# Kernel tuning notes

Hardware: AMD Instinct MI355X
Metric: run time of the kernel (lower is better)

The kernel has to match this reference:

```python
import jax, jax.numpy as jnp
import numpy as np

B, S, H, MID = 8, 2048, 256, 32


def get_rotary_matrix(s, d):
    # Faithful to llama-from-scratch get_rotary_matrix: theta = 10000**(-2*(i-1)/d)
    pos = jnp.arange(s, dtype=jnp.float32)
    i = jnp.arange(d // 2, dtype=jnp.float32)
    theta = 10000.0 ** (-2.0 * (i - 1.0) / d)
    ang = pos[:, None] * theta[None, :]            # [s, d/2]
    c, sn = jnp.cos(ang), jnp.sin(ang)
    ev = 2 * jnp.arange(d // 2)
    od = ev + 1
    R = jnp.zeros((s, d, d), jnp.float32)
    R = R.at[:, ev, ev].set(c).at[:, od, od].set(c)
    R = R.at[:, ev, od].set(-sn).at[:, od, ev].set(sn)
    return R


def setup_inputs() -> dict:
    key = jax.random.key(0)
    ks = jax.random.split(key, 7)
    sc = 0.02
    x = jax.random.normal(ks[0], (B, S, H), jnp.float32)
    # nn.Linear weights: l1.weight [mid, in], l2.weight [out, mid]; y = x @ W.T
    wq1 = jax.random.normal(ks[1], (MID, H), jnp.float32) * sc
    wq2 = jax.random.normal(ks[2], (H, MID), jnp.float32) * sc
    wk1 = jax.random.normal(ks[3], (MID, H), jnp.float32) * sc
    wk2 = jax.random.normal(ks[4], (H, MID), jnp.float32) * sc
    wv1 = jax.random.normal(ks[5], (MID, H), jnp.float32) * sc
    wv2 = jax.random.normal(ks[6], (H, MID), jnp.float32) * sc
    r = get_rotary_matrix(S, H)                    # [S, H, H] buffer
    return {"x": x, "r": r, "wq1": wq1, "wq2": wq2, "wk1": wk1,
            "wk2": wk2, "wv1": wv1, "wv2": wv2}


def reference(x, r, wq1, wq2, wk1, wk2, wv1, wv2):
    b, s, h = x.shape
    q = (x @ wq1.T) @ wq2.T                        # LoRA q: [b,s,h]
    k = (x @ wk1.T) @ wk2.T
    v = (x @ wv1.T) @ wv2.T
    # RoPE as dense per-position rotation matmul (bmm over seq dim)
    qr = jnp.einsum('bsh,shk->bsk', q, r[:s])
    kr = jnp.einsum('bsh,shk->bsk', k, r[:s])
    attn = jnp.einsum('bqh,bkh->bqk', qr, kr) * (h ** -0.5)   # [b,s,s]
    mask = jnp.tril(jnp.ones((s, s), bool))
    attn = jnp.where(mask, attn, -jnp.inf)
    attn = jax.nn.softmax(attn, axis=-1)
    out = attn @ v                                 # [b,s,h]
    return out
```

## Files before the change

kernel.cpp:

```cpp
#include <hip/hip_runtime.h>
#include <hip/hip_bf16.h>
#include <math.h>

typedef float f32x4 __attribute__((ext_vector_type(4)));
typedef float f32x16 __attribute__((ext_vector_type(16)));
typedef unsigned int u32x4 __attribute__((ext_vector_type(4)));
typedef __bf16 bf16x8 __attribute__((ext_vector_type(8)));
typedef unsigned short u16;

#define MFMA16(acc, a, b)                                              \
  acc = __builtin_amdgcn_mfma_f32_16x16x32_bf16(                       \
      __builtin_bit_cast(bf16x8, a), __builtin_bit_cast(bf16x8, b),    \
      acc, 0, 0, 0)

#define MFMA32(acc, a, b)                                              \
  acc = __builtin_amdgcn_mfma_f32_32x32x16_bf16(                       \
      __builtin_bit_cast(bf16x8, a), __builtin_bit_cast(bf16x8, b),    \
      acc, 0, 0, 0)

#define GLOAD_LDS16(gp, lp)                                            \
  __builtin_amdgcn_global_load_lds(                                    \
      (const __attribute__((address_space(1))) void*)(const void*)(gp),\
      (__attribute__((address_space(3))) void*)(void*)(lp), 16, 0, 0)

__device__ __forceinline__ u16 f2bf(float f) {
  union { float f; unsigned u; } v; v.f = f;
  unsigned r = v.u + 0x7FFFu + ((v.u >> 16) & 1u);
  return (u16)(r >> 16);
}

__device__ __forceinline__ float b2f(u16 h) {
  union { unsigned u; float f; } v; v.u = ((unsigned)h) << 16; return v.f;
}

__device__ __forceinline__ unsigned cvtpk(float lo, float hi) {
  unsigned r;
  asm("v_cvt_pk_bf16_f32 %0, %1, %2" : "=v"(r) : "v"(lo), "v"(hi));
  return r;
}

#define BFEX(vec, e) ((u16)(((e) & 1) ? ((vec)[(e) >> 1] >> 16) : ((vec)[(e) >> 1] & 0xffffu)))

__global__ __launch_bounds__(256) void cs_kernel(float2* __restrict__ cs) {
  int idx = blockIdx.x * 256 + threadIdx.x;
  int s = idx >> 7, j = idx & 127;
  float theta = powf(10000.f, (2.f - 2.f * (float)j) * (1.f / 256.f));
  float ang = (float)s * theta;
  float sn, c;
  sincosf(ang, &sn, &c);
  cs[idx] = make_float2(c, sn);
}

__global__ __launch_bounds__(256) void proj_kernel(
    const float* __restrict__ x,
    const float* __restrict__ w1q, const float* __restrict__ w2q,
    const float* __restrict__ w1k, const float* __restrict__ w2k,
    const float* __restrict__ w1v, const float* __restrict__ w2v,
    const float2* __restrict__ cs,
    u16* __restrict__ qout, u16* __restrict__ kout, u16* __restrict__ vout)
{
  __shared__ __align__(16) u16 xs[64 * 256];
  __shared__ __align__(16) u16 w1s[32 * 256];
  __shared__ __align__(16) u16 w2s[256 * 40];
  __shared__ __align__(16) u16 tls[64 * 40];
  __shared__ __align__(16) u16 bnc[64 * 264];

  const int tid = threadIdx.x;
  const int w = tid >> 6, l = tid & 63;
  const int l15 = l & 15, lg = l >> 4;
  const int row0 = blockIdx.x * 64;

  #pragma unroll
  for (int i = 0; i < 16; ++i) {
    int idx = tid + 256 * i;
    int r = idx >> 6, c4 = idx & 63;
    float4 v = reinterpret_cast<const float4*>(x)[(size_t)(row0 + r) * 64 + c4];
    int ci = (c4 * 4) ^ ((r & 7) << 3);
    *reinterpret_cast<ushort4*>(&xs[r * 256 + ci]) =
        make_ushort4(f2bf(v.x), f2bf(v.y), f2bf(v.z), f2bf(v.w));
  }

  const float* W1[3] = {w1q, w1k, w1v};
  const float* W2[3] = {w2q, w2k, w2v};
  u16* OUT[3] = {qout, kout, vout};

  for (int p = 0; p < 3; ++p) {
    __syncthreads();
    const float* w1 = W1[p];
    const float* w2 = W2[p];
    #pragma unroll
    for (int i = 0; i < 8; ++i) {
      int idx = tid + 256 * i;
      int r = idx >> 6, c4 = idx & 63;
      float4 v = reinterpret_cast<const float4*>(w1)[idx];
      int ci = (c4 * 4) ^ ((r & 7) << 3);
      *reinterpret_cast<ushort4*>(&w1s[r * 256 + ci]) =
          make_ushort4(f2bf(v.x), f2bf(v.y), f2bf(v.z), f2bf(v.w));
    }
    #pragma unroll
    for (int i = 0; i < 8; ++i) {
      int idx = tid + 256 * i;
      int r = idx >> 3, c4 = idx & 7;
      float4 v = reinterpret_cast<const float4*>(w2)[idx];
      *reinterpret_cast<ushort4*>(&w2s[r * 40 + c4 * 4]) =
          make_ushort4(f2bf(v.x), f2bf(v.y), f2bf(v.z), f2bf(v.w));
    }
    __syncthreads();

    f32x4 acc0 = {0.f, 0.f, 0.f, 0.f}, acc1 = {0.f, 0.f, 0.f, 0.f};
    {
      const int arow = w * 16 + l15;
      #pragma unroll
      for (int kk = 0; kk < 8; ++kk) {
        u32x4 a = *reinterpret_cast<const u32x4*>(
            &xs[arow * 256 + ((kk * 32 + lg * 8) ^ ((arow & 7) << 3))]);
        const int b0r = l15, b1r = l15 + 16;
        u32x4 b0 = *reinterpret_cast<const u32x4*>(
            &w1s[b0r * 256 + ((kk * 32 + lg * 8) ^ ((b0r & 7) << 3))]);
        u32x4 b1 = *reinterpret_cast<const u32x4*>(
            &w1s[b1r * 256 + ((kk * 32 + lg * 8) ^ ((b1r & 7) << 3))]);
        MFMA16(acc0, a, b0);
        MFMA16(acc1, a, b1);
      }
    }
    #pragma unroll
    for (int rr = 0; rr < 4; ++rr) {
      int trow = w * 16 + lg * 4 + rr;
      tls[trow * 40 + l15]      = f2bf(acc0[rr]);
      tls[trow * 40 + 16 + l15] = f2bf(acc1[rr]);
    }

    f32x4 yac[16];
    #pragma unroll
    for (int oc = 0; oc < 16; ++oc) yac[oc] = (f32x4){0.f, 0.f, 0.f, 0.f};
    {
      u32x4 a = *reinterpret_cast<const u32x4*>(&tls[(w * 16 + l15) * 40 + lg * 8]);
      #pragma unroll
      for (int oc = 0; oc < 16; ++oc) {
        u32x4 b = *reinterpret_cast<const u32x4*>(&w2s[(oc * 16 + l15) * 40 + lg * 8]);
        MFMA16(yac[oc], a, b);
      }
    }

    #pragma unroll
    for (int oc = 0; oc < 16; ++oc)
      #pragma unroll
      for (int rr = 0; rr < 4; ++rr)
        bnc[(w * 16 + lg * 4 + rr) * 264 + oc * 16 + l15] = f2bf(yac[oc][rr]);
    __syncthreads();

    {
      const int frow = tid >> 2, c0 = (tid & 3) * 64;
      const int grow = row0 + frow;
      const int sidx = grow & 2047;
      u16* outp = OUT[p];
      const float2* csr = cs + ((size_t)sidx << 7) + (c0 >> 1);
      const bool dorope = (p < 2);
      #pragma unroll
      for (int seg = 0; seg < 8; ++seg) {
        u32x4 v8 = *reinterpret_cast<const u32x4*>(&bnc[frow * 264 + c0 + seg * 8]);
        u32x4 res = v8;
        if (dorope) {
          #pragma unroll
          for (int j = 0; j < 4; ++j) {
            float ev = b2f(BFEX(v8, 2 * j)), od = b2f(BFEX(v8, 2 * j + 1));
            float2 cv = csr[seg * 4 + j];
            u16 re = f2bf(ev * cv.x + od * cv.y);
            u16 ro = f2bf(od * cv.x - ev * cv.y);
            res[j] = ((unsigned)ro << 16) | (unsigned)re;
          }
        }
        *reinterpret_cast<u32x4*>(&outp[(size_t)grow * 256 + c0 + seg * 8]) = res;
      }
    }
  }
}

__global__ __launch_bounds__(256, 2) void attn_kernel(
    const u16* __restrict__ qg, const u16* __restrict__ kg,
    const u16* __restrict__ vg, u16* __restrict__ po,
    float* __restrict__ pmw, float* __restrict__ plw)
{
  __shared__ __align__(16) u16 ks2[2][32 * 256];
  __shared__ __align__(16) u16 vt2[2][256 * 40];
  __shared__ float paxw[4][32];

  const int tid = threadIdx.x;
  const int w = tid >> 6, l = tid & 63;
  const int s = w >> 1, h2 = w & 1;
  const int q31 = l & 31, g = l >> 5;

  const int bx = blockIdx.x;
  const int bb = bx & 7;
  const int o_ = bx >> 3;
  const int idx = (o_ < 32) ? o_ : 95 - o_;
  const int qt = 31 - (idx >> 1);
  const int hv = idx & 1;
  const int tmx = 2 * qt + 1;

  const int qbase = qt * 64;
  const size_t boff = (size_t)bb * (2048 * 256);
  const int qg_ = qbase + s * 32 + q31;

  u32x4 qf[16];
  {
    const u16* qp = qg + boff + (size_t)qg_ * 256 + g * 8;
    #pragma unroll
    for (int st = 0; st < 16; ++st)
      qf[st] = *reinterpret_cast<const u32x4*>(qp + st * 16);
  }

  f32x16 o[4];
  #pragma unroll
  for (int dt = 0; dt < 4; ++dt)
    #pragma unroll
    for (int r = 0; r < 16; ++r) o[dt][r] = 0.f;
  float m_run = -INFINITY, l_run = 0.f;

  const int vc = tid & 31;
  const int kvr = (tid >> 5) * 4;
  const int swv = (vc & 3) << 3;
  const int swr = (q31 >> 3) << 3;
  const int ksw = (q31 & 7) << 3;
  const int kbase = q31 * 256;

  const u16* kgb = kg + boff;
  const u16* vgb = vg + boff;

  {
    const u16* kp = kgb + (size_t)(hv * 32) * 256;
    #pragma unroll
    for (int j = 0; j < 4; ++j) {
      int i2 = tid + 256 * j;
      int r = i2 >> 5, c8 = (i2 & 31) * 8;
      GLOAD_LDS16(kp + r * 256 + (c8 ^ ((r & 7) << 3)), &ks2[0][i2 * 8]);
    }
    const u16* vp = vgb + (size_t)(hv * 32) * 256;
    u32x4 vq[4];
    #pragma unroll
    for (int j = 0; j < 4; ++j)
      vq[j] = *reinterpret_cast<const u32x4*>(vp + (size_t)(kvr + j) * 256 + vc * 8);
    #pragma unroll
    for (int e = 0; e < 8; ++e) {
      int d = vc * 8 + e;
      *reinterpret_cast<ushort4*>(&vt2[0][d * 40 + (kvr ^ swv)]) =
          make_ushort4(BFEX(vq[0], e), BFEX(vq[1], e), BFEX(vq[2], e), BFEX(vq[3], e));
    }
  }
  __syncthreads();

  int cur = 0;
  for (int t = hv; t <= tmx; t += 2) {
    const int kv0 = t * 32;
    const int nb = cur ^ 1;
    const bool pf = (t + 2 <= tmx);

    u32x4 vq[4];
    if (pf) {
      const u16* kp = kgb + (size_t)((t + 2) * 32) * 256;
      #pragma unroll
      for (int j = 0; j < 4; ++j) {
        int i2 = tid + 256 * j;
        int r = i2 >> 5, c8 = (i2 & 31) * 8;
        GLOAD_LDS16(kp + r * 256 + (c8 ^ ((r & 7) << 3)), &ks2[nb][i2 * 8]);
      }
      const u16* vp = vgb + (size_t)((t + 2) * 32) * 256;
      #pragma unroll
      for (int j = 0; j < 4; ++j)
        vq[j] = *reinterpret_cast<const u32x4*>(vp + (size_t)(kvr + j) * 256 + vc * 8);
    }

    f32x16 sca, scb;
    #pragma unroll
    for (int r = 0; r < 16; ++r) { sca[r] = 0.f; scb[r] = 0.f; }
    #pragma unroll
    for (int st = 0; st < 8; ++st) {
      u32x4 a0 = *reinterpret_cast<const u32x4*>(
          &ks2[cur][kbase + ((st * 32 + g * 8) ^ ksw)]);
      u32x4 a1 = *reinterpret_cast<const u32x4*>(
          &ks2[cur][kbase + ((st * 32 + 16 + g * 8) ^ ksw)]);
      MFMA32(sca, a0, qf[2 * st]);
      MFMA32(scb, a1, qf[2 * st + 1]);
    }

    f32x16 sc;
    #pragma unroll
    for (int r = 0; r < 16; ++r) sc[r] = (sca[r] + scb[r]) * 0.0625f;
    if (kv0 + 31 > qbase + s * 32) {
      #pragma unroll
      for (int r = 0; r < 16; ++r) {
        int kvg = kv0 + (r & 3) + 8 * (r >> 2) + 4 * g;
        if (kvg > qg_) sc[r] = -INFINITY;
      }
    }
    float red[8];
    #pragma unroll
    for (int i = 0; i < 8; ++i) red[i] = fmaxf(sc[i], sc[i + 8]);
    #pragma unroll
    for (int i = 0; i < 4; ++i) red[i] = fmaxf(red[i], red[i + 4]);
    float mx = fmaxf(fmaxf(red[0], red[1]), fmaxf(red[2], red[3]));
    mx = fmaxf(mx, __shfl_xor(mx, 32, 64));
    float mnew = fmaxf(m_run, mx);
    float msafe = fmaxf(mnew, -1e30f);
    float alpha = __expf(m_run - msafe);
    m_run = mnew;
    #pragma unroll
    for (int r = 0; r < 16; ++r) sc[r] = __expf(sc[r] - msafe);
    #pragma unroll
    for (int i = 0; i < 8; ++i) red[i] = sc[i] + sc[i + 8];
    #pragma unroll
    for (int i = 0; i < 4; ++i) red[i] = red[i] + red[i + 4];
    float lh = (red[0] + red[1]) + (red[2] + red[3]);
    lh += __shfl_xor(lh, 32, 64);
    l_run = l_run * alpha + lh;

    unsigned wv[8], xw[8];
    #pragma unroll
    for (int j = 0; j < 8; ++j) wv[j] = cvtpk(sc[2 * j], sc[2 * j + 1]);
    #pragma unroll
    for (int j = 0; j < 8; ++j) xw[j] = __shfl_xor(wv[j], 32, 64);
    u32x4 pa0, pa1;
    pa0[0] = g ? xw[2] : wv[0]; pa0[1] = g ? xw[3] : wv[1];
    pa0[2] = g ? wv[2] : xw[0]; pa0[3] = g ? wv[3] : xw[1];
    pa1[0] = g ? xw[6] : wv[4]; pa1[1] = g ? xw[7] : wv[5];
    pa1[2] = g ? wv[6] : xw[4]; pa1[3] = g ? wv[7] : xw[5];

    if (l < 32) paxw[w][l] = alpha;
    f32x4 aR[4];
    #pragma unroll
    for (int i = 0; i < 4; ++i)
      aR[i] = *reinterpret_cast<const f32x4*>(&paxw[w][i * 8 + 4 * g]);
    #pragma unroll
    for (int dt = 0; dt < 4; ++dt)
      #pragma unroll
      for (int r = 0; r < 16; ++r) o[dt][r] *= aR[r >> 2][r & 3];

    #pragma unroll
    for (int dt = 0; dt < 4; ++dt) {
      int rb = (h2 * 128 + dt * 32 + q31) * 40;
      u32x4 b0 = *reinterpret_cast<const u32x4*>(&vt2[cur][rb + ((g * 8) ^ swr)]);
      u32x4 b1 = *reinterpret_cast<const u32x4*>(&vt2[cur][rb + ((16 + g * 8) ^ swr)]);
      MFMA32(o[dt], pa0, b0);
      MFMA32(o[dt], pa1, b1);
    }

    if (pf) {
      #pragma unroll
      for (int e = 0; e < 8; ++e) {
        int d = vc * 8 + e;
        *reinterpret_cast<ushort4*>(&vt2[nb][d * 40 + (kvr ^ swv)]) =
            make_ushort4(BFEX(vq[0], e), BFEX(vq[1], e), BFEX(vq[2], e), BFEX(vq[3], e));
      }
    }
    __syncthreads();
    cur ^= 1;
  }

  const int pidx = (bb * 32 + qt) * 2 + hv;
  u16* op = po + (size_t)pidx * (64 * 256);
  #pragma unroll
  for (int dt = 0; dt < 4; ++dt) {
    #pragma unroll
    for (int r = 0; r < 16; ++r) {
      int row = s * 32 + (r & 3) + 8 * (r >> 2) + 4 * g;
      int col = h2 * 128 + dt * 32 + q31;
      op[(size_t)row * 256 + col] = f2bf(o[dt][r]);
    }
  }
  if (h2 == 0 && l < 32) {
    pmw[pidx * 64 + s * 32 + l] = m_run;
    plw[pidx * 64 + s * 32 + l] = l_run;
  }
}

__global__ __launch_bounds__(256) void combine_kernel(
    const u16* __restrict__ po, const float* __restrict__ pm,
    const float* __restrict__ plv, float* __restrict__ outg)
{
  int idx = blockIdx.x * 256 + threadIdx.x;
  int d8 = idx & 31;
  int row = idx >> 5;
  int bb = row >> 11, qrem = row & 2047;
  int qt = qrem >> 6, r64 = qrem & 63;
  int p0 = (bb * 32 + qt) * 2;

  float m0 = pm[p0 * 64 + r64], m1 = pm[(p0 + 1) * 64 + r64];
  float l0 = plv[p0 * 64 + r64], l1 = plv[(p0 + 1) * 64 + r64];
  float mm = fmaxf(m0, m1);
  float w0 = __expf(m0 - mm), w1 = __expf(m1 - mm);
  float inv = 1.f / (l0 * w0 + l1 * w1);

  u32x4 a0 = *reinterpret_cast<const u32x4*>(
      po + (size_t)p0 * (64 * 256) + (size_t)r64 * 256 + d8 * 8);
  u32x4 a1 = *reinterpret_cast<const u32x4*>(
      po + (size_t)(p0 + 1) * (64 * 256) + (size_t)r64 * 256 + d8 * 8);
  f32x4 r0, r1;
  #pragma unroll
  for (int e = 0; e < 4; ++e)
    r0[e] = (b2f(BFEX(a0, e)) * w0 + b2f(BFEX(a1, e)) * w1) * inv;
  #pragma unroll
  for (int e = 0; e < 4; ++e)
    r1[e] = (b2f(BFEX(a0, e + 4)) * w0 + b2f(BFEX(a1, e + 4)) * w1) * inv;
  float* op = outg + (size_t)row * 256 + d8 * 8;
  *reinterpret_cast<f32x4*>(op) = r0;
  *reinterpret_cast<f32x4*>(op + 4) = r1;
}

extern "C" void kernel_launch(void* const* d_in, const int* in_sizes, int n_in,
                              void* d_out, int out_size, void* d_ws, size_t ws_size,
                              hipStream_t stream) {
  const float* x   = (const float*)d_in[0];
  const float* wq1 = (const float*)d_in[2];
  const float* wq2 = (const float*)d_in[3];
  const float* wk1 = (const float*)d_in[4];
  const float* wk2 = (const float*)d_in[5];
  const float* wv1 = (const float*)d_in[6];
  const float* wv2 = (const float*)d_in[7];

  const size_t NTOK = (size_t)8 * 2048;
  u16* qw = (u16*)d_ws;
  u16* kw = qw + NTOK * 256;
  u16* vw = kw + NTOK * 256;
  float2* cs = (float2*)(vw + NTOK * 256);
  u16* po    = (u16*)(cs + 2048 * 128);
  float* pm  = (float*)(po + (size_t)512 * 64 * 256);
  float* plv = pm + 512 * 64;

  cs_kernel<<<1024, 256, 0, stream>>>(cs);
  proj_kernel<<<256, 256, 0, stream>>>(x, wq1, wq2, wk1, wk2, wv1, wv2,
                                       cs, qw, kw, vw);
  attn_kernel<<<512, 256, 0, stream>>>(qw, kw, vw, po, pm, plv);
  combine_kernel<<<2048, 256, 0, stream>>>(po, pm, plv, (float*)d_out);
}
```

Baseline: 109.1 us.

## Split KV into four strided partitions with atomic work-queue scheduling in attention

The attention kernel becomes persistent. Each block pulls work items from a per-batch atomic counter, which is reset in cs_kernel, and the item order runs longest tiles first. The KV range of each query tile is split four ways instead of two, and the combine kernel merges four partial softmax results. It also skips the output rescale when alpha equals 1 across the wave. This is meant to improve load balance in causal attention, at the cost of more partial-output traffic, a larger combine step and atomic/sync overhead per item.

```diff
diff --git a/kernel.cpp b/kernel.cpp
--- a/kernel.cpp
+++ b/kernel.cpp
@@ -41,8 +41,10 @@
 
 #define BFEX(vec, e) ((u16)(((e) & 1) ? ((vec)[(e) >> 1] >> 16) : ((vec)[(e) >> 1] & 0xffffu)))
 
-__global__ __launch_bounds__(256) void cs_kernel(float2* __restrict__ cs) {
+__global__ __launch_bounds__(256) void cs_kernel(float2* __restrict__ cs,
+                                                 int* __restrict__ ctr) {
   int idx = blockIdx.x * 256 + threadIdx.x;
+  if (blockIdx.x == 0 && threadIdx.x < 8) ctr[threadIdx.x] = 0;
   int s = idx >> 7, j = idx & 127;
   float theta = powf(10000.f, (2.f - 2.f * (float)j) * (1.f / 256.f));
   float ang = (float)s * theta;
@@ -179,43 +181,22 @@
 __global__ __launch_bounds__(256, 2) void attn_kernel(
     const u16* __restrict__ qg, const u16* __restrict__ kg,
     const u16* __restrict__ vg, u16* __restrict__ po,
-    float* __restrict__ pmw, float* __restrict__ plw)
+    float* __restrict__ pmw, float* __restrict__ plw, int* __restrict__ ctr)
 {
   __shared__ __align__(16) u16 ks2[2][32 * 256];
   __shared__ __align__(16) u16 vt2[2][256 * 40];
   __shared__ float paxw[4][32];
+  __shared__ int s_item;
 
   const int tid = threadIdx.x;
   const int w = tid >> 6, l = tid & 63;
   const int s = w >> 1, h2 = w & 1;
   const int q31 = l & 31, g = l >> 5;
 
-  const int bx = blockIdx.x;
-  const int bb = bx & 7;
-  const int o_ = bx >> 3;
-  const int idx = (o_ < 32) ? o_ : 95 - o_;
-  const int qt = 31 - (idx >> 1);
-  const int hv = idx & 1;
-  const int tmx = 2 * qt + 1;
-
-  const int qbase = qt * 64;
+  const int bb = blockIdx.x & 7;
   const size_t boff = (size_t)bb * (2048 * 256);
-  const int qg_ = qbase + s * 32 + q31;
-
-  u32x4 qf[16];
-  {
-    const u16* qp = qg + boff + (size_t)qg_ * 256 + g * 8;
-    #pragma unroll
-    for (int st = 0; st < 16; ++st)
-      qf[st] = *reinterpret_cast<const u32x4*>(qp + st * 16);
-  }
-
-  f32x16 o[4];
-  #pragma unroll
-  for (int dt = 0; dt < 4; ++dt)
-    #pragma unroll
-    for (int r = 0; r < 16; ++r) o[dt][r] = 0.f;
-  float m_run = -INFINITY, l_run = 0.f;
+  const u16* kgb = kg + boff;
+  const u16* vgb = vg + boff;
 
   const int vc = tid & 31;
   const int kvr = (tid >> 5) * 4;
@@ -224,152 +205,182 @@
   const int ksw = (q31 & 7) << 3;
   const int kbase = q31 * 256;
 
-  const u16* kgb = kg + boff;
-  const u16* vgb = vg + boff;
-
-  {
-    const u16* kp = kgb + (size_t)(hv * 32) * 256;
-    #pragma unroll
-    for (int j = 0; j < 4; ++j) {
-      int i2 = tid + 256 * j;
-      int r = i2 >> 5, c8 = (i2 & 31) * 8;
-      GLOAD_LDS16(kp + r * 256 + (c8 ^ ((r & 7) << 3)), &ks2[0][i2 * 8]);
-    }
-    const u16* vp = vgb + (size_t)(hv * 32) * 256;
-    u32x4 vq[4];
-    #pragma unroll
-    for (int j = 0; j < 4; ++j)
-      vq[j] = *reinterpret_cast<const u32x4*>(vp + (size_t)(kvr + j) * 256 + vc * 8);
-    #pragma unroll
-    for (int e = 0; e < 8; ++e) {
-      int d = vc * 8 + e;
-      *reinterpret_cast<ushort4*>(&vt2[0][d * 40 + (kvr ^ swv)]) =
-          make_ushort4(BFEX(vq[0], e), BFEX(vq[1], e), BFEX(vq[2], e), BFEX(vq[3], e));
-    }
-  }
-  __syncthreads();
-
-  int cur = 0;
-  for (int t = hv; t <= tmx; t += 2) {
-    const int kv0 = t * 32;
-    const int nb = cur ^ 1;
-    const bool pf = (t + 2 <= tmx);
-
-    u32x4 vq[4];
-    if (pf) {
-      const u16* kp = kgb + (size_t)((t + 2) * 32) * 256;
-      #pragma unroll
-      for (int j = 0; j < 4; ++j) {
-        int i2 = tid + 256 * j;
-        int r = i2 >> 5, c8 = (i2 & 31) * 8;
-        GLOAD_LDS16(kp + r * 256 + (c8 ^ ((r & 7) << 3)), &ks2[nb][i2 * 8]);
-      }
-      const u16* vp = vgb + (size_t)((t + 2) * 32) * 256;
-      #pragma unroll
-      for (int j = 0; j < 4; ++j)
-        vq[j] = *reinterpret_cast<const u32x4*>(vp + (size_t)(kvr + j) * 256 + vc * 8);
-    }
-
-    f32x16 sca, scb;
-    #pragma unroll
-    for (int r = 0; r < 16; ++r) { sca[r] = 0.f; scb[r] = 0.f; }
-    #pragma unroll
-    for (int st = 0; st < 8; ++st) {
-      u32x4 a0 = *reinterpret_cast<const u32x4*>(
-          &ks2[cur][kbase + ((st * 32 + g * 8) ^ ksw)]);
-      u32x4 a1 = *reinterpret_cast<const u32x4*>(
-          &ks2[cur][kbase + ((st * 32 + 16 + g * 8) ^ ksw)]);
-      MFMA32(sca, a0, qf[2 * st]);
-      MFMA32(scb, a1, qf[2 * st + 1]);
-    }
-
-    f32x16 sc;
-    #pragma unroll
-    for (int r = 0; r < 16; ++r) sc[r] = (sca[r] + scb[r]) * 0.0625f;
-    if (kv0 + 31 > qbase + s * 32) {
+  for (;;) {
+    if (tid == 0) s_item = atomicAdd(&ctr[bb], 1);
+    __syncthreads();
+    const int it = s_item;
+    __syncthreads();
+    if (it >= 128) break;
+
+    const int qt = 31 - (it >> 2);
+    const int hv = it & 3;
+    const int tmx = 2 * qt + 1;
+    const int qbase = qt * 64;
+    const int qg_ = qbase + s * 32 + q31;
+
+    u32x4 qf[16];
+    {
+      const u16* qp = qg + boff + (size_t)qg_ * 256 + g * 8;
+      #pragma unroll
+      for (int st = 0; st < 16; ++st)
+        qf[st] = *reinterpret_cast<const u32x4*>(qp + st * 16);
+    }
+
+    f32x16 o[4];
+    #pragma unroll
+    for (int dt = 0; dt < 4; ++dt)
+      #pragma unroll
+      for (int r = 0; r < 16; ++r) o[dt][r] = 0.f;
+    float m_run = -INFINITY, l_run = 0.f;
+
+    if (hv <= tmx) {
+      {
+        const u16* kp = kgb + (size_t)(hv * 32) * 256;
+        #pragma unroll
+        for (int j = 0; j < 4; ++j) {
+          int i2 = tid + 256 * j;
+          int r = i2 >> 5, c8 = (i2 & 31) * 8;
+          GLOAD_LDS16(kp + r * 256 + (c8 ^ ((r & 7) << 3)), &ks2[0][i2 * 8]);
+        }
+        const u16* vp = vgb + (size_t)(hv * 32) * 256;
+        u32x4 vq[4];
+        #pragma unroll
+        for (int j = 0; j < 4; ++j)
+          vq[j] = *reinterpret_cast<const u32x4*>(vp + (size_t)(kvr + j) * 256 + vc * 8);
+        #pragma unroll
+        for (int e = 0; e < 8; ++e) {
+          int d = vc * 8 + e;
+          *reinterpret_cast<ushort4*>(&vt2[0][d * 40 + (kvr ^ swv)]) =
+              make_ushort4(BFEX(vq[0], e), BFEX(vq[1], e), BFEX(vq[2], e), BFEX(vq[3], e));
+        }
+      }
+      __syncthreads();
+
+      int cur = 0;
+      for (int t = hv; t <= tmx; t += 4) {
+        const int kv0 = t * 32;
+        const int nb = cur ^ 1;
+        const bool pf = (t + 4 <= tmx);
+
+        u32x4 vq[4];
+        if (pf) {
+          const u16* kp = kgb + (size_t)((t + 4) * 32) * 256;
+          #pragma unroll
+          for (int j = 0; j < 4; ++j) {
+            int i2 = tid + 256 * j;
+            int r = i2 >> 5, c8 = (i2 & 31) * 8;
+            GLOAD_LDS16(kp + r * 256 + (c8 ^ ((r & 7) << 3)), &ks2[nb][i2 * 8]);
+          }
+          const u16* vp = vgb + (size_t)((t + 4) * 32) * 256;
+          #pragma unroll
+          for (int j = 0; j < 4; ++j)
+            vq[j] = *reinterpret_cast<const u32x4*>(vp + (size_t)(kvr + j) * 256 + vc * 8);
+        }
+
+        f32x16 sca, scb;
+        #pragma unroll
+        for (int r = 0; r < 16; ++r) { sca[r] = 0.f; scb[r] = 0.f; }
+        #pragma unroll
+        for (int st = 0; st < 8; ++st) {
+          u32x4 a0 = *reinterpret_cast<const u32x4*>(
+              &ks2[cur][kbase + ((st * 32 + g * 8) ^ ksw)]);
+          u32x4 a1 = *reinterpret_cast<const u32x4*>(
+              &ks2[cur][kbase + ((st * 32 + 16 + g * 8) ^ ksw)]);
+          MFMA32(sca, a0, qf[2 * st]);
+          MFMA32(scb, a1, qf[2 * st + 1]);
+        }
+
+        f32x16 sc;
+        #pragma unroll
+        for (int r = 0; r < 16; ++r) sc[r] = (sca[r] + scb[r]) * 0.0625f;
+        if (kv0 + 31 > qbase + s * 32) {
+          #pragma unroll
+          for (int r = 0; r < 16; ++r) {
+            int kvg = kv0 + (r & 3) + 8 * (r >> 2) + 4 * g;
+            if (kvg > qg_) sc[r] = -INFINITY;
+          }
+        }
+        float red[8];
+        #pragma unroll
+        for (int i = 0; i < 8; ++i) red[i] = fmaxf(sc[i], sc[i + 8]);
+        #pragma unroll
+        for (int i = 0; i < 4; ++i) red[i] = fmaxf(red[i], red[i + 4]);
+        float mx = fmaxf(fmaxf(red[0], red[1]), fmaxf(red[2], red[3]));
+        mx = fmaxf(mx, __shfl_xor(mx, 32, 64));
+        float mnew = fmaxf(m_run, mx);
+        float msafe = fmaxf(mnew, -1e30f);
+        float alpha = __expf(m_run - msafe);
+        m_run = mnew;
+        #pragma unroll
+        for (int r = 0; r < 16; ++r) sc[r] = __expf(sc[r] - msafe);
+        #pragma unroll
+        for (int i = 0; i < 8; ++i) red[i] = sc[i] + sc[i + 8];
+        #pragma unroll
+        for (int i = 0; i < 4; ++i) red[i] = red[i] + red[i + 4];
+        float lh = (red[0] + red[1]) + (red[2] + red[3]);
+        lh += __shfl_xor(lh, 32, 64);
+        l_run = l_run * alpha + lh;
+
+        unsigned wv[8], xw[8];
+        #pragma unroll
+        for (int j = 0; j < 8; ++j) wv[j] = cvtpk(sc[2 * j], sc[2 * j + 1]);
+        #pragma unroll
+        for (int j = 0; j < 8; ++j) xw[j] = __shfl_xor(wv[j], 32, 64);
+        u32x4 pa0, pa1;
+        pa0[0] = g ? xw[2] : wv[0]; pa0[1] = g ? xw[3] : wv[1];
+        pa0[2] = g ? wv[2] : xw[0]; pa0[3] = g ? wv[3] : xw[1];
+        pa1[0] = g ? xw[6] : wv[4]; pa1[1] = g ? xw[7] : wv[5];
+        pa1[2] = g ? wv[6] : xw[4]; pa1[3] = g ? wv[7] : xw[5];
+
+        if (!__all(alpha == 1.0f)) {
+          if (l < 32) paxw[w][l] = alpha;
+          f32x4 aR[4];
+          #pragma unroll
+          for (int i = 0; i < 4; ++i)
+            aR[i] = *reinterpret_cast<const f32x4*>(&paxw[w][i * 8 + 4 * g]);
+          #pragma unroll
+          for (int dt = 0; dt < 4; ++dt)
+            #pragma unroll
+            for (int r = 0; r < 16; ++r) o[dt][r] *= aR[r >> 2][r & 3];
+        }
+
+        #pragma unroll
+        for (int dt = 0; dt < 4; ++dt) {
+          int rb = (h2 * 128 + dt * 32 + q31) * 40;
+          u32x4 b0 = *reinterpret_cast<const u32x4*>(&vt2[cur][rb + ((g * 8) ^ swr)]);
+          u32x4 b1 = *reinterpret_cast<const u32x4*>(&vt2[cur][rb + ((16 + g * 8) ^ swr)]);
+          MFMA32(o[dt], pa0, b0);
+          MFMA32(o[dt], pa1, b1);
+        }
+
+        if (pf) {
+          #pragma unroll
+          for (int e = 0; e < 8; ++e) {
+            int d = vc * 8 + e;
+            *reinterpret_cast<ushort4*>(&vt2[nb][d * 40 + (kvr ^ swv)]) =
+                make_ushort4(BFEX(vq[0], e), BFEX(vq[1], e), BFEX(vq[2], e), BFEX(vq[3], e));
+          }
+        }
+        __syncthreads();
+        cur ^= 1;
+      }
+    }
+
+    const int pidx = (bb * 32 + qt) * 4 + hv;
+    u16* op = po + (size_t)pidx * (64 * 256);
+    #pragma unroll
+    for (int dt = 0; dt < 4; ++dt) {
       #pragma unroll
       for (int r = 0; r < 16; ++r) {
-        int kvg = kv0 + (r & 3) + 8 * (r >> 2) + 4 * g;
-        if (kvg > qg_) sc[r] = -INFINITY;
-      }
-    }
-    float red[8];
-    #pragma unroll
-    for (int i = 0; i < 8; ++i) red[i] = fmaxf(sc[i], sc[i + 8]);
-    #pragma unroll
-    for (int i = 0; i < 4; ++i) red[i] = fmaxf(red[i], red[i + 4]);
-    float mx = fmaxf(fmaxf(red[0], red[1]), fmaxf(red[2], red[3]));
-    mx = fmaxf(mx, __shfl_xor(mx, 32, 64));
-    float mnew = fmaxf(m_run, mx);
-    float msafe = fmaxf(mnew, -1e30f);
-    float alpha = __expf(m_run - msafe);
-    m_run = mnew;
-    #pragma unroll
-    for (int r = 0; r < 16; ++r) sc[r] = __expf(sc[r] - msafe);
-    #pragma unroll
-    for (int i = 0; i < 8; ++i) red[i] = sc[i] + sc[i + 8];
-    #pragma unroll
-    for (int i = 0; i < 4; ++i) red[i] = red[i] + red[i + 4];
-    float lh = (red[0] + red[1]) + (red[2] + red[3]);
-    lh += __shfl_xor(lh, 32, 64);
-    l_run = l_run * alpha + lh;
-
-    unsigned wv[8], xw[8];
-    #pragma unroll
-    for (int j = 0; j < 8; ++j) wv[j] = cvtpk(sc[2 * j], sc[2 * j + 1]);
-    #pragma unroll
-    for (int j = 0; j < 8; ++j) xw[j] = __shfl_xor(wv[j], 32, 64);
-    u32x4 pa0, pa1;
-    pa0[0] = g ? xw[2] : wv[0]; pa0[1] = g ? xw[3] : wv[1];
-    pa0[2] = g ? wv[2] : xw[0]; pa0[3] = g ? wv[3] : xw[1];
-    pa1[0] = g ? xw[6] : wv[4]; pa1[1] = g ? xw[7] : wv[5];
-    pa1[2] = g ? wv[6] : xw[4]; pa1[3] = g ? wv[7] : xw[5];
-
-    if (l < 32) paxw[w][l] = alpha;
-    f32x4 aR[4];
-    #pragma unroll
-    for (int i = 0; i < 4; ++i)
-      aR[i] = *reinterpret_cast<const f32x4*>(&paxw[w][i * 8 + 4 * g]);
-    #pragma unroll
-    for (int dt = 0; dt < 4; ++dt)
-      #pragma unroll
-      for (int r = 0; r < 16; ++r) o[dt][r] *= aR[r >> 2][r & 3];
-
-    #pragma unroll
-    for (int dt = 0; dt < 4; ++dt) {
-      int rb = (h2 * 128 + dt * 32 + q31) * 40;
-      u32x4 b0 = *reinterpret_cast<const u32x4*>(&vt2[cur][rb + ((g * 8) ^ swr)]);
-      u32x4 b1 = *reinterpret_cast<const u32x4*>(&vt2[cur][rb + ((16 + g * 8) ^ swr)]);
-      MFMA32(o[dt], pa0, b0);
-      MFMA32(o[dt], pa1, b1);
-    }
-
-    if (pf) {
-      #pragma unroll
-      for (int e = 0; e < 8; ++e) {
-        int d = vc * 8 + e;
-        *reinterpret_cast<ushort4*>(&vt2[nb][d * 40 + (kvr ^ swv)]) =
-            make_ushort4(BFEX(vq[0], e), BFEX(vq[1], e), BFEX(vq[2], e), BFEX(vq[3], e));
-      }
-    }
-    __syncthreads();
-    cur ^= 1;
-  }
-
-  const int pidx = (bb * 32 + qt) * 2 + hv;
-  u16* op = po + (size_t)pidx * (64 * 256);
-  #pragma unroll
-  for (int dt = 0; dt < 4; ++dt) {
-    #pragma unroll
-    for (int r = 0; r < 16; ++r) {
-      int row = s * 32 + (r & 3) + 8 * (r >> 2) + 4 * g;
-      int col = h2 * 128 + dt * 32 + q31;
-      op[(size_t)row * 256 + col] = f2bf(o[dt][r]);
-    }
-  }
-  if (h2 == 0 && l < 32) {
-    pmw[pidx * 64 + s * 32 + l] = m_run;
-    plw[pidx * 64 + s * 32 + l] = l_run;
+        int row = s * 32 + (r & 3) + 8 * (r >> 2) + 4 * g;
+        int col = h2 * 128 + dt * 32 + q31;
+        op[(size_t)row * 256 + col] = f2bf(o[dt][r]);
+      }
+    }
+    if (h2 == 0 && l < 32) {
+      pmw[pidx * 64 + s * 32 + l] = m_run;
+      plw[pidx * 64 + s * 32 + l] = l_run;
+    }
   }
 }
 
@@ -382,25 +393,36 @@
   int row = idx >> 5;
   int bb = row >> 11, qrem = row & 2047;
   int qt = qrem >> 6, r64 = qrem & 63;
-  int p0 = (bb * 32 + qt) * 2;
-
-  float m0 = pm[p0 * 64 + r64], m1 = pm[(p0 + 1) * 64 + r64];
-  float l0 = plv[p0 * 64 + r64], l1 = plv[(p0 + 1) * 64 + r64];
-  float mm = fmaxf(m0, m1);
-  float w0 = __expf(m0 - mm), w1 = __expf(m1 - mm);
-  float inv = 1.f / (l0 * w0 + l1 * w1);
-
-  u32x4 a0 = *reinterpret_cast<const u32x4*>(
-      po + (size_t)p0 * (64 * 256) + (size_t)r64 * 256 + d8 * 8);
-  u32x4 a1 = *reinterpret_cast<const u32x4*>(
-      po + (size_t)(p0 + 1) * (64 * 256) + (size_t)r64 * 256 + d8 * 8);
-  f32x4 r0, r1;
+  int p0 = (bb * 32 + qt) * 4;
+
+  float mj[4], lj[4];
   #pragma unroll
-  for (int e = 0; e < 4; ++e)
-    r0[e] = (b2f(BFEX(a0, e)) * w0 + b2f(BFEX(a1, e)) * w1) * inv;
+  for (int j = 0; j < 4; ++j) {
+    mj[j] = pm[(p0 + j) * 64 + r64];
+    lj[j] = plv[(p0 + j) * 64 + r64];
+  }
+  float mm = fmaxf(fmaxf(mj[0], mj[1]), fmaxf(mj[2], mj[3]));
+  float wj[4];
+  float den = 0.f;
   #pragma unroll
-  for (int e = 0; e < 4; ++e)
-    r1[e] = (b2f(BFEX(a0, e + 4)) * w0 + b2f(BFEX(a1, e + 4)) * w1) * inv;
+  for (int j = 0; j < 4; ++j) {
+    wj[j] = __expf(mj[j] - mm);
+    den += lj[j] * wj[j];
+  }
+  float inv = 1.f / den;
+
+  f32x4 r0 = {0.f, 0.f, 0.f, 0.f}, r1 = {0.f, 0.f, 0.f, 0.f};
+  #pragma unroll
+  for (int j = 0; j < 4; ++j) {
+    u32x4 a = *reinterpret_cast<const u32x4*>(
+        po + (size_t)(p0 + j) * (64 * 256) + (size_t)r64 * 256 + d8 * 8);
+    #pragma unroll
+    for (int e = 0; e < 4; ++e) r0[e] += b2f(BFEX(a, e)) * wj[j];
+    #pragma unroll
+    for (int e = 0; e < 4; ++e) r1[e] += b2f(BFEX(a, e + 4)) * wj[j];
+  }
+  #pragma unroll
+  for (int e = 0; e < 4; ++e) { r0[e] *= inv; r1[e] *= inv; }
   float* op = outg + (size_t)row * 256 + d8 * 8;
   *reinterpret_cast<f32x4*>(op) = r0;
   *reinterpret_cast<f32x4*>(op + 4) = r1;
@@ -423,12 +445,13 @@
   u16* vw = kw + NTOK * 256;
   float2* cs = (float2*)(vw + NTOK * 256);
   u16* po    = (u16*)(cs + 2048 * 128);
-  float* pm  = (float*)(po + (size_t)512 * 64 * 256);
-  float* plv = pm + 512 * 64;
-
-  cs_kernel<<<1024, 256, 0, stream>>>(cs);
+  float* pm  = (float*)(po + (size_t)1024 * 64 * 256);
+  float* plv = pm + 1024 * 64;
+  int* ctr   = (int*)(plv + 1024 * 64);
+
+  cs_kernel<<<1024, 256, 0, stream>>>(cs, ctr);
   proj_kernel<<<256, 256, 0, stream>>>(x, wq1, wq2, wk1, wk2, wv1, wv2,
                                        cs, qw, kw, vw);
-  attn_kernel<<<512, 256, 0, stream>>>(qw, kw, vw, po, pm, plv);
+  attn_kernel<<<512, 256, 0, stream>>>(qw, kw, vw, po, pm, plv, ctr);
   combine_kernel<<<2048, 256, 0, stream>>>(po, pm, plv, (float*)d_out);
 }
```

New measurement: 123.9 us. 13.6% more time.

## Load K fragments directly from global memory and skip rescale when max unchanged

Applied to the files above, without the earlier changes.

The double-buffered LDS staging of K tiles (global_load_lds plus swizzled LDS reads) is removed. Each lane now loads its K MFMA operand fragments straight from global/L2 into registers in two batches of eight. This frees LDS and removes the LDS round trip, at the cost of more global traffic and load latency exposed right before the QK MFMAs. It also adds a wave-uniform skip of the output rescale when every alpha equals one.

```diff
diff --git a/kernel.cpp b/kernel.cpp
--- a/kernel.cpp
+++ b/kernel.cpp
@@ -17,11 +17,6 @@
   acc = __builtin_amdgcn_mfma_f32_32x32x16_bf16(                       \
       __builtin_bit_cast(bf16x8, a), __builtin_bit_cast(bf16x8, b),    \
       acc, 0, 0, 0)
-
-#define GLOAD_LDS16(gp, lp)                                            \
-  __builtin_amdgcn_global_load_lds(                                    \
-      (const __attribute__((address_space(1))) void*)(const void*)(gp),\
-      (__attribute__((address_space(3))) void*)(void*)(lp), 16, 0, 0)
 
 __device__ __forceinline__ u16 f2bf(float f) {
   union { float f; unsigned u; } v; v.f = f;
@@ -181,7 +176,6 @@
     const u16* __restrict__ vg, u16* __restrict__ po,
     float* __restrict__ pmw, float* __restrict__ plw)
 {
-  __shared__ __align__(16) u16 ks2[2][32 * 256];
   __shared__ __align__(16) u16 vt2[2][256 * 40];
   __shared__ float paxw[4][32];
 
@@ -221,20 +215,12 @@
   const int kvr = (tid >> 5) * 4;
   const int swv = (vc & 3) << 3;
   const int swr = (q31 >> 3) << 3;
-  const int ksw = (q31 & 7) << 3;
-  const int kbase = q31 * 256;
 
   const u16* kgb = kg + boff;
   const u16* vgb = vg + boff;
+  const u16* krb = kgb + (size_t)q31 * 256 + g * 8;
 
   {
-    const u16* kp = kgb + (size_t)(hv * 32) * 256;
-    #pragma unroll
-    for (int j = 0; j < 4; ++j) {
-      int i2 = tid + 256 * j;
-      int r = i2 >> 5, c8 = (i2 & 31) * 8;
-      GLOAD_LDS16(kp + r * 256 + (c8 ^ ((r & 7) << 3)), &ks2[0][i2 * 8]);
-    }
     const u16* vp = vgb + (size_t)(hv * 32) * 256;
     u32x4 vq[4];
     #pragma unroll
@@ -257,30 +243,30 @@
 
     u32x4 vq[4];
     if (pf) {
-      const u16* kp = kgb + (size_t)((t + 2) * 32) * 256;
-      #pragma unroll
-      for (int j = 0; j < 4; ++j) {
-        int i2 = tid + 256 * j;
-        int r = i2 >> 5, c8 = (i2 & 31) * 8;
-        GLOAD_LDS16(kp + r * 256 + (c8 ^ ((r & 7) << 3)), &ks2[nb][i2 * 8]);
-      }
       const u16* vp = vgb + (size_t)((t + 2) * 32) * 256;
       #pragma unroll
       for (int j = 0; j < 4; ++j)
         vq[j] = *reinterpret_cast<const u32x4*>(vp + (size_t)(kvr + j) * 256 + vc * 8);
     }
 
+    const u16* kr = krb + (size_t)kv0 * 256;
     f32x16 sca, scb;
     #pragma unroll
     for (int r = 0; r < 16; ++r) { sca[r] = 0.f; scb[r] = 0.f; }
-    #pragma unroll
-    for (int st = 0; st < 8; ++st) {
-      u32x4 a0 = *reinterpret_cast<const u32x4*>(
-          &ks2[cur][kbase + ((st * 32 + g * 8) ^ ksw)]);
-      u32x4 a1 = *reinterpret_cast<const u32x4*>(
-          &ks2[cur][kbase + ((st * 32 + 16 + g * 8) ^ ksw)]);
-      MFMA32(sca, a0, qf[2 * st]);
-      MFMA32(scb, a1, qf[2 * st + 1]);
+    {
+      u32x4 kf[8];
+      #pragma unroll
+      for (int m = 0; m < 8; ++m)
+        kf[m] = *reinterpret_cast<const u32x4*>(kr + m * 16);
+      #pragma unroll
+      for (int m = 0; m < 8; ++m)
+        MFMA32((m & 1) ? scb : sca, kf[m], qf[m]);
+      #pragma unroll
+      for (int m = 0; m < 8; ++m)
+        kf[m] = *reinterpret_cast<const u32x4*>(kr + 128 + m * 16);
+      #pragma unroll
+      for (int m = 0; m < 8; ++m)
+        MFMA32((m & 1) ? scb : sca, kf[m], qf[m + 8]);
     }
 
     f32x16 sc;
@@ -325,15 +311,17 @@
     pa1[0] = g ? xw[6] : wv[4]; pa1[1] = g ? xw[7] : wv[5];
     pa1[2] = g ? wv[6] : xw[4]; pa1[3] = g ? wv[7] : xw[5];
 
-    if (l < 32) paxw[w][l] = alpha;
-    f32x4 aR[4];
-    #pragma unroll
-    for (int i = 0; i < 4; ++i)
-      aR[i] = *reinterpret_cast<const f32x4*>(&paxw[w][i * 8 + 4 * g]);
-    #pragma unroll
-    for (int dt = 0; dt < 4; ++dt)
-      #pragma unroll
-      for (int r = 0; r < 16; ++r) o[dt][r] *= aR[r >> 2][r & 3];
+    if (!__all(alpha == 1.0f)) {
+      if (l < 32) paxw[w][l] = alpha;
+      f32x4 aR[4];
+      #pragma unroll
+      for (int i = 0; i < 4; ++i)
+        aR[i] = *reinterpret_cast<const f32x4*>(&paxw[w][i * 8 + 4 * g]);
+      #pragma unroll
+      for (int dt = 0; dt < 4; ++dt)
+        #pragma unroll
+        for (int r = 0; r < 16; ++r) o[dt][r] *= aR[r >> 2][r & 3];
+    }
 
     #pragma unroll
     for (int dt = 0; dt < 4; ++dt) {
```

Result: slower. 127.4 us (+16.8%).

## Split projections across grid, compute RoPE inline, skip unit-alpha rescale

Applied to the files above, without the earlier changes.

The projection kernel now launches a 3-wide grid so each block handles a single Q/K/V projection instead of looping over all three, which triples the block count. Shared memory is aliased so the output staging buffer reuses the x tile, lowering per-block LDS. The separate cos/sin table kernel is dropped and the rotary angles are computed inline with exp2 and sincos, removing one launch and the table traffic. In the attention loop, the output rescale is skipped when every lane's alpha equals one. In exchange, x is loaded and converted three times, the RoPE path does more transcendental math, and the rescale check adds a wave vote.

```diff
diff --git a/kernel.cpp b/kernel.cpp
--- a/kernel.cpp
+++ b/kernel.cpp
@@ -41,34 +41,30 @@
 
 #define BFEX(vec, e) ((u16)(((e) & 1) ? ((vec)[(e) >> 1] >> 16) : ((vec)[(e) >> 1] & 0xffffu)))
 
-__global__ __launch_bounds__(256) void cs_kernel(float2* __restrict__ cs) {
-  int idx = blockIdx.x * 256 + threadIdx.x;
-  int s = idx >> 7, j = idx & 127;
-  float theta = powf(10000.f, (2.f - 2.f * (float)j) * (1.f / 256.f));
-  float ang = (float)s * theta;
-  float sn, c;
-  sincosf(ang, &sn, &c);
-  cs[idx] = make_float2(c, sn);
-}
-
 __global__ __launch_bounds__(256) void proj_kernel(
     const float* __restrict__ x,
     const float* __restrict__ w1q, const float* __restrict__ w2q,
     const float* __restrict__ w1k, const float* __restrict__ w2k,
     const float* __restrict__ w1v, const float* __restrict__ w2v,
-    const float2* __restrict__ cs,
     u16* __restrict__ qout, u16* __restrict__ kout, u16* __restrict__ vout)
 {
-  __shared__ __align__(16) u16 xs[64 * 256];
-  __shared__ __align__(16) u16 w1s[32 * 256];
-  __shared__ __align__(16) u16 w2s[256 * 40];
-  __shared__ __align__(16) u16 tls[64 * 40];
-  __shared__ __align__(16) u16 bnc[64 * 264];
+  __shared__ __align__(16) u16 smem[37376];
+  u16* xs  = smem;
+  u16* w1s = smem + 16384;
+  u16* w2s = smem + 24576;
+  u16* tls = smem + 34816;
+  u16* bnc = smem;
 
   const int tid = threadIdx.x;
   const int w = tid >> 6, l = tid & 63;
   const int l15 = l & 15, lg = l >> 4;
   const int row0 = blockIdx.x * 64;
+  const int p = blockIdx.y;
+
+  const float* w1 = (p == 0) ? w1q : (p == 1) ? w1k : w1v;
+  const float* w2 = (p == 0) ? w2q : (p == 1) ? w2k : w2v;
+  u16* outp = (p == 0) ? qout : (p == 1) ? kout : vout;
+  const bool dorope = (p < 2);
 
   #pragma unroll
   for (int i = 0; i < 16; ++i) {
@@ -79,99 +75,93 @@
     *reinterpret_cast<ushort4*>(&xs[r * 256 + ci]) =
         make_ushort4(f2bf(v.x), f2bf(v.y), f2bf(v.z), f2bf(v.w));
   }
-
-  const float* W1[3] = {w1q, w1k, w1v};
-  const float* W2[3] = {w2q, w2k, w2v};
-  u16* OUT[3] = {qout, kout, vout};
-
-  for (int p = 0; p < 3; ++p) {
-    __syncthreads();
-    const float* w1 = W1[p];
-    const float* w2 = W2[p];
-    #pragma unroll
-    for (int i = 0; i < 8; ++i) {
-      int idx = tid + 256 * i;
-      int r = idx >> 6, c4 = idx & 63;
-      float4 v = reinterpret_cast<const float4*>(w1)[idx];
-      int ci = (c4 * 4) ^ ((r & 7) << 3);
-      *reinterpret_cast<ushort4*>(&w1s[r * 256 + ci]) =
-          make_ushort4(f2bf(v.x), f2bf(v.y), f2bf(v.z), f2bf(v.w));
-    }
-    #pragma unroll
-    for (int i = 0; i < 8; ++i) {
-      int idx = tid + 256 * i;
-      int r = idx >> 3, c4 = idx & 7;
-      float4 v = reinterpret_cast<const float4*>(w2)[idx];
-      *reinterpret_cast<ushort4*>(&w2s[r * 40 + c4 * 4]) =
-          make_ushort4(f2bf(v.x), f2bf(v.y), f2bf(v.z), f2bf(v.w));
-    }
-    __syncthreads();
-
-    f32x4 acc0 = {0.f, 0.f, 0.f, 0.f}, acc1 = {0.f, 0.f, 0.f, 0.f};
-    {
-      const int arow = w * 16 + l15;
-      #pragma unroll
-      for (int kk = 0; kk < 8; ++kk) {
-        u32x4 a = *reinterpret_cast<const u32x4*>(
-            &xs[arow * 256 + ((kk * 32 + lg * 8) ^ ((arow & 7) << 3))]);
-        const int b0r = l15, b1r = l15 + 16;
-        u32x4 b0 = *reinterpret_cast<const u32x4*>(
-            &w1s[b0r * 256 + ((kk * 32 + lg * 8) ^ ((b0r & 7) << 3))]);
-        u32x4 b1 = *reinterpret_cast<const u32x4*>(
-            &w1s[b1r * 256 + ((kk * 32 + lg * 8) ^ ((b1r & 7) << 3))]);
-        MFMA16(acc0, a, b0);
-        MFMA16(acc1, a, b1);
+  #pragma unroll
+  for (int i = 0; i < 8; ++i) {
+    int idx = tid + 256 * i;
+    int r = idx >> 6, c4 = idx & 63;
+    float4 v = reinterpret_cast<const float4*>(w1)[idx];
+    int ci = (c4 * 4) ^ ((r & 7) << 3);
+    *reinterpret_cast<ushort4*>(&w1s[r * 256 + ci]) =
+        make_ushort4(f2bf(v.x), f2bf(v.y), f2bf(v.z), f2bf(v.w));
+  }
+  #pragma unroll
+  for (int i = 0; i < 8; ++i) {
+    int idx = tid + 256 * i;
+    int r = idx >> 3, c4 = idx & 7;
+    float4 v = reinterpret_cast<const float4*>(w2)[idx];
+    *reinterpret_cast<ushort4*>(&w2s[r * 40 + c4 * 4]) =
+        make_ushort4(f2bf(v.x), f2bf(v.y), f2bf(v.z), f2bf(v.w));
+  }
+  __syncthreads();
+
+  f32x4 acc0 = {0.f, 0.f, 0.f, 0.f}, acc1 = {0.f, 0.f, 0.f, 0.f};
+  {
+    const int arow = w * 16 + l15;
+    #pragma unroll
+    for (int kk = 0; kk < 8; ++kk) {
+      u32x4 a = *reinterpret_cast<const u32x4*>(
+          &xs[arow * 256 + ((kk * 32 + lg * 8) ^ ((arow & 7) << 3))]);
+      const int b0r = l15, b1r = l15 + 16;
+      u32x4 b0 = *reinterpret_cast<const u32x4*>(
+          &w1s[b0r * 256 + ((kk * 32 + lg * 8) ^ ((b0r & 7) << 3))]);
+      u32x4 b1 = *reinterpret_cast<const u32x4*>(
+          &w1s[b1r * 256 + ((kk * 32 + lg * 8) ^ ((b1r & 7) << 3))]);
+      MFMA16(acc0, a, b0);
+      MFMA16(acc1, a, b1);
+    }
+  }
+  #pragma unroll
+  for (int rr = 0; rr < 4; ++rr) {
+    int trow = w * 16 + lg * 4 + rr;
+    tls[trow * 40 + l15]      = f2bf(acc0[rr]);
+    tls[trow * 40 + 16 + l15] = f2bf(acc1[rr]);
+  }
+
+  f32x4 yac[16];
+  #pragma unroll
+  for (int oc = 0; oc < 16; ++oc) yac[oc] = (f32x4){0.f, 0.f, 0.f, 0.f};
+  {
+    u32x4 a = *reinterpret_cast<const u32x4*>(&tls[(w * 16 + l15) * 40 + lg * 8]);
+    #pragma unroll
+    for (int oc = 0; oc < 16; ++oc) {
+      u32x4 b = *reinterpret_cast<const u32x4*>(&w2s[(oc * 16 + l15) * 40 + lg * 8]);
+      MFMA16(yac[oc], a, b);
+    }
+  }
+  __syncthreads();
+
+  #pragma unroll
+  for (int oc = 0; oc < 16; ++oc)
+    #pragma unroll
+    for (int rr = 0; rr < 4; ++rr)
+      bnc[(w * 16 + lg * 4 + rr) * 264 + oc * 16 + l15] = f2bf(yac[oc][rr]);
+  __syncthreads();
+
+  {
+    const int frow = tid >> 2, c0 = (tid & 3) * 64;
+    const int grow = row0 + frow;
+    const int sidx = grow & 2047;
+    const float sfl = (float)sidx;
+    #pragma unroll
+    for (int seg = 0; seg < 8; ++seg) {
+      u32x4 v8 = *reinterpret_cast<const u32x4*>(&bnc[frow * 264 + c0 + seg * 8]);
+      u32x4 res = v8;
+      if (dorope) {
+        #pragma unroll
+        for (int j = 0; j < 4; ++j) {
+          int jp = (c0 >> 1) + seg * 4 + j;
+          float theta = __builtin_exp2f(13.287712379549449f *
+                                        (2.f - 2.f * (float)jp) * (1.f / 256.f));
+          float ang = sfl * theta;
+          float sn, c;
+          sincosf(ang, &sn, &c);
+          float ev = b2f(BFEX(v8, 2 * j)), od = b2f(BFEX(v8, 2 * j + 1));
+          u16 re = f2bf(ev * c + od * sn);
+          u16 ro = f2bf(od * c - ev * sn);
+          res[j] = ((unsigned)ro << 16) | (unsigned)re;
+        }
       }
-    }
-    #pragma unroll
-    for (int rr = 0; rr < 4; ++rr) {
-      int trow = w * 16 + lg * 4 + rr;
-      tls[trow * 40 + l15]      = f2bf(acc0[rr]);
-      tls[trow * 40 + 16 + l15] = f2bf(acc1[rr]);
-    }
-
-    f32x4 yac[16];
-    #pragma unroll
-    for (int oc = 0; oc < 16; ++oc) yac[oc] = (f32x4){0.f, 0.f, 0.f, 0.f};
-    {
-      u32x4 a = *reinterpret_cast<const u32x4*>(&tls[(w * 16 + l15) * 40 + lg * 8]);
-      #pragma unroll
-      for (int oc = 0; oc < 16; ++oc) {
-        u32x4 b = *reinterpret_cast<const u32x4*>(&w2s[(oc * 16 + l15) * 40 + lg * 8]);
-        MFMA16(yac[oc], a, b);
-      }
-    }
-
-    #pragma unroll
-    for (int oc = 0; oc < 16; ++oc)
-      #pragma unroll
-      for (int rr = 0; rr < 4; ++rr)
-        bnc[(w * 16 + lg * 4 + rr) * 264 + oc * 16 + l15] = f2bf(yac[oc][rr]);
-    __syncthreads();
-
-    {
-      const int frow = tid >> 2, c0 = (tid & 3) * 64;
-      const int grow = row0 + frow;
-      const int sidx = grow & 2047;
-      u16* outp = OUT[p];
-      const float2* csr = cs + ((size_t)sidx << 7) + (c0 >> 1);
-      const bool dorope = (p < 2);
-      #pragma unroll
-      for (int seg = 0; seg < 8; ++seg) {
-        u32x4 v8 = *reinterpret_cast<const u32x4*>(&bnc[frow * 264 + c0 + seg * 8]);
-        u32x4 res = v8;
-        if (dorope) {
-          #pragma unroll
-          for (int j = 0; j < 4; ++j) {
-            float ev = b2f(BFEX(v8, 2 * j)), od = b2f(BFEX(v8, 2 * j + 1));
-            float2 cv = csr[seg * 4 + j];
-            u16 re = f2bf(ev * cv.x + od * cv.y);
-            u16 ro = f2bf(od * cv.x - ev * cv.y);
-            res[j] = ((unsigned)ro << 16) | (unsigned)re;
-          }
-        }
-        *reinterpret_cast<u32x4*>(&outp[(size_t)grow * 256 + c0 + seg * 8]) = res;
-      }
+      *reinterpret_cast<u32x4*>(&outp[(size_t)grow * 256 + c0 + seg * 8]) = res;
     }
   }
 }
@@ -325,15 +315,17 @@
     pa1[0] = g ? xw[6] : wv[4]; pa1[1] = g ? xw[7] : wv[5];
     pa1[2] = g ? wv[6] : xw[4]; pa1[3] = g ? wv[7] : xw[5];
 
-    if (l < 32) paxw[w][l] = alpha;
-    f32x4 aR[4];
-    #pragma unroll
-    for (int i = 0; i < 4; ++i)
-      aR[i] = *reinterpret_cast<const f32x4*>(&paxw[w][i * 8 + 4 * g]);
-    #pragma unroll
-    for (int dt = 0; dt < 4; ++dt)
-      #pragma unroll
-      for (int r = 0; r < 16; ++r) o[dt][r] *= aR[r >> 2][r & 3];
+    if (!__all(alpha == 1.0f)) {
+      if (l < 32) paxw[w][l] = alpha;
+      f32x4 aR[4];
+      #pragma unroll
+      for (int i = 0; i < 4; ++i)
+        aR[i] = *reinterpret_cast<const f32x4*>(&paxw[w][i * 8 + 4 * g]);
+      #pragma unroll
+      for (int dt = 0; dt < 4; ++dt)
+        #pragma unroll
+        for (int r = 0; r < 16; ++r) o[dt][r] *= aR[r >> 2][r & 3];
+    }
 
     #pragma unroll
     for (int dt = 0; dt < 4; ++dt) {
@@ -421,14 +413,12 @@
   u16* qw = (u16*)d_ws;
   u16* kw = qw + NTOK * 256;
   u16* vw = kw + NTOK * 256;
-  float2* cs = (float2*)(vw + NTOK * 256);
-  u16* po    = (u16*)(cs + 2048 * 128);
+  u16* po = vw + NTOK * 256;
   float* pm  = (float*)(po + (size_t)512 * 64 * 256);
   float* plv = pm + 512 * 64;
 
-  cs_kernel<<<1024, 256, 0, stream>>>(cs);
-  proj_kernel<<<256, 256, 0, stream>>>(x, wq1, wq2, wk1, wk2, wv1, wv2,
-                                       cs, qw, kw, vw);
+  proj_kernel<<<dim3(256, 3), 256, 0, stream>>>(x, wq1, wq2, wk1, wk2, wv1, wv2,
+                                                qw, kw, vw);
   attn_kernel<<<512, 256, 0, stream>>>(qw, kw, vw, po, pm, plv);
   combine_kernel<<<2048, 256, 0, stream>>>(po, pm, plv, (float*)d_out);
 }
```

Measured after the change: 94.62 us (median of 2 runs). 1.15x faster.
